# Optimization experiments

Measured on AMD Instinct MI355X. Metric: run time of the kernel, lower is better.

## Reference

```python
import jax, jax.numpy as jnp
import numpy as np

D, NH, DH, DHR, DC = 2048, 16, 128, 64, 1024
B, L = 2, 2048
EPS = 1e-6


def _rms(x, w):
    return x * jax.lax.rsqrt(jnp.mean(x * x, axis=-1, keepdims=True) + EPS) * w


def _rope_tables(seq_len, dim, dtype):
    inv_freq = 1.0 / (10000.0 ** (jnp.arange(0, dim, 2, dtype=jnp.float32) / dim))
    freqs = jnp.arange(seq_len, dtype=jnp.float32)[:, None] * inv_freq[None, :]  # [L, dim/2]
    emb = jnp.concatenate([freqs, freqs], axis=-1)                               # [L, dim]
    return jnp.cos(emb).astype(dtype), jnp.sin(emb).astype(dtype)


def _apply_rope(x, cos, sin):
    # x: [B, H, L, dhr]
    half = x.shape[-1] // 2
    x1, x2 = x[..., :half], x[..., half:]
    rot = jnp.concatenate([-x2, x1], axis=-1)
    return x * cos[None, None] + rot * sin[None, None]


def setup_inputs() -> dict:
    key = jax.random.key(0)
    ks = jax.random.split(key, 14)
    s = 0.02
    inp = {
        "x": jax.random.normal(ks[0], (B, L, D), dtype=jnp.float32),
        "W_DKV": jax.random.normal(ks[1], (D, DC), dtype=jnp.float32) * s,
        "kv_norm_w": 1.0 + 0.01 * jax.random.normal(ks[2], (DC,), dtype=jnp.float32),
        "W_UK": jax.random.normal(ks[3], (DC, NH * DH), dtype=jnp.float32) * s,
        "W_UV": jax.random.normal(ks[4], (DC, NH * DH), dtype=jnp.float32) * s,
        "W_DQ": jax.random.normal(ks[5], (D, DC), dtype=jnp.float32) * s,
        "q_norm_w": 1.0 + 0.01 * jax.random.normal(ks[6], (DC,), dtype=jnp.float32),
        "W_UQ": jax.random.normal(ks[7], (DC, 2 * NH * DH), dtype=jnp.float32) * s,
        "W_QR": jax.random.normal(ks[8], (DC, 2 * NH * DHR), dtype=jnp.float32) * s,
        "W_KR": jax.random.normal(ks[9], (D, DHR), dtype=jnp.float32) * s,
        "W_lambda_w": jax.random.normal(ks[10], (D, NH), dtype=jnp.float32) * s,
        "W_lambda_b": jax.random.normal(ks[11], (NH,), dtype=jnp.float32) * s,
        "W_out": jax.random.normal(ks[12], (D, D), dtype=jnp.float32) * s,
    }
    return inp


def reference(x, W_DKV, kv_norm_w, W_UK, W_UV, W_DQ, q_norm_w, W_UQ, W_QR,
              W_KR, W_lambda_w, W_lambda_b, W_out):
    Bx, Lx, Dx = x.shape
    nh, dh, dhr = NH, DH, DHR
    dq = dh + dhr  # per-head query/key dim after decoupled-RoPE concat (192)
    scale = 1.0 / jnp.sqrt(jnp.asarray(dq, dtype=x.dtype))

    # MLA KV path
    c_kv = _rms(x @ W_DKV, kv_norm_w)                                   # [B,L,dc]
    k_c = (c_kv @ W_UK).reshape(Bx, Lx, nh, dh).transpose(0, 2, 1, 3)    # [B,nh,L,dh]
    v = (c_kv @ W_UV).reshape(Bx, Lx, nh, dh).transpose(0, 2, 1, 3)      # [B,nh,L,dh]

    # MLA Q path (doubled heads for Diff V2)
    c_q = _rms(x @ W_DQ, q_norm_w)                                       # [B,L,dcq]
    q_c = (c_q @ W_UQ).reshape(Bx, Lx, 2 * nh, dh).transpose(0, 2, 1, 3)  # [B,2nh,L,dh]

    # Decoupled RoPE
    cos, sin = _rope_tables(Lx, dhr, x.dtype)
    q_r = _apply_rope((c_q @ W_QR).reshape(Bx, Lx, 2 * nh, dhr).transpose(0, 2, 1, 3), cos, sin)
    k_r = _apply_rope((x @ W_KR).reshape(Bx, Lx, 1, dhr).transpose(0, 2, 1, 3), cos, sin)  # [B,1,L,dhr]

    q = jnp.concatenate([q_c, q_r], axis=-1)                             # [B,2nh,L,dq]
    k = jnp.concatenate([k_c, jnp.broadcast_to(k_r, (Bx, nh, Lx, dhr))], axis=-1)  # [B,nh,L,dq]

    # repeat_interleave(2) on K/V == pairing two consecutive Q heads with one K/V head
    qp = q.reshape(Bx, nh, 2, Lx, dq)                                    # [B,nh,2,L,dq]
    scores = jnp.einsum('bnpld,bnmd->bnplm', qp, k) * scale              # [B,nh,2,L,L]
    causal = jnp.tril(jnp.ones((Lx, Lx), dtype=bool))
    scores = jnp.where(causal[None, None, None], scores, jnp.finfo(scores.dtype).min)
    p = jax.nn.softmax(scores, axis=-1)
    attn = jnp.einsum('bnplm,bnmd->bnpld', p, v)                         # [B,nh,2,L,dh]

    attn1, attn2 = attn[:, :, 0], attn[:, :, 1]                          # [B,nh,L,dh]
    lam = jax.nn.sigmoid(x @ W_lambda_w + W_lambda_b)                    # [B,L,nh]
    lam = lam.transpose(0, 2, 1)[..., None]                              # [B,nh,L,1]
    out = (attn1 - lam * attn2).transpose(0, 2, 1, 3).reshape(Bx, Lx, Dx)
    return out @ W_out
```

## Files before the change

### kernel.cpp

```cpp
#include <hip/hip_runtime.h>
#include <cstddef>
#include <cstdint>


namespace {

constexpr int kDC = 1024, kDim = 2048;
constexpr float kScale = 0.07216878364870323f;
constexpr int kTA = 2128;

typedef __bf16 bf16x8 __attribute__((ext_vector_type(8)));
typedef float f32x4 __attribute__((ext_vector_type(4)));

__device__ __forceinline__ unsigned short f2bf(float f) {
  __bf16 h = (__bf16)f;
  return __builtin_bit_cast(unsigned short, h);
}
__device__ __forceinline__ float bf2f(unsigned short h) {
  union { unsigned int u; float f; } v; v.u = ((unsigned int)h) << 16;
  return v.f;
}
__device__ __forceinline__ f32x4 mfma16(bf16x8 a, bf16x8 b, f32x4 c) {
  return __builtin_amdgcn_mfma_f32_16x16x32_bf16(a, b, c, 0, 0, 0);
}
__device__ __forceinline__ void gl_lds16(const void* g, void* l) {
  __builtin_amdgcn_global_load_lds(
      (const __attribute__((address_space(1))) unsigned int*)g,
      (__attribute__((address_space(3))) unsigned int*)l, 16, 0, 0);
}
__device__ __forceinline__ void wait_lgkm0() {
  asm volatile("s_waitcnt lgkmcnt(0)" ::: "memory");
}

__global__ __launch_bounds__(256) void conv_bf16_kernel(const float* __restrict__ in,
                                                        unsigned short* __restrict__ out, int n4) {
  int e = blockIdx.x * 256 + threadIdx.x;
  if (e >= n4) return;
  float4 v = reinterpret_cast<const float4*>(in)[e];
  uint2 pk;
  pk.x = (unsigned int)f2bf(v.x) | ((unsigned int)f2bf(v.y) << 16);
  pk.y = (unsigned int)f2bf(v.z) | ((unsigned int)f2bf(v.w) << 16);
  reinterpret_cast<uint2*>(out)[e] = pk;
}

__global__ __launch_bounds__(256) void zero_bf16_kernel(unsigned short* __restrict__ out, int n8) {
  int e = blockIdx.x * 256 + threadIdx.x;
  if (e >= n8) return;
  reinterpret_cast<uint4*>(out)[e] = uint4{0, 0, 0, 0};
}

__global__ __launch_bounds__(256) void transpose_conv_kernel(const float* __restrict__ in,
                                                             unsigned short* __restrict__ out,
                                                             int K, int N) {
  __shared__ float t[32][33];
  int n0 = blockIdx.x * 32, k0 = blockIdx.y * 32;
  int tx = threadIdx.x & 31, ty = threadIdx.x >> 5;
#pragma unroll
  for (int i = 0; i < 4; i++) t[ty + i * 8][tx] = in[(size_t)(k0 + ty + i * 8) * N + n0 + tx];
  __syncthreads();
#pragma unroll
  for (int i = 0; i < 4; i++)
    out[(size_t)(n0 + ty + i * 8) * K + k0 + tx] = f2bf(t[tx][ty + i * 8]);
}

__global__ __launch_bounds__(256) void lamw_transpose_kernel(const float* __restrict__ in,
                                                             unsigned short* __restrict__ out) {
  int e = blockIdx.x * 256 + threadIdx.x;
  if (e >= 16 * 2048) return;
  int k = e & 2047, n = e >> 11;
  out[(size_t)(2112 + n) * 2048 + k] = f2bf(in[(size_t)k * 16 + n]);
}

template <int MODE>
__device__ __forceinline__ void epi_store(void* dst, void* dst2, int gr, int gc, int N, float v) {
  if (MODE == 0) {
    reinterpret_cast<float*>(dst)[(size_t)gr * N + gc] = v;
  } else if (MODE == 4) {
    if (gc < kTA) reinterpret_cast<float*>(dst)[(size_t)gr * kTA + gc] = v;
  } else if (MODE == 5) {
    int bb = gr >> 11, l = gr & 2047;
    unsigned short hv = f2bf(v);
    if (gc < 2048) {
      int h = gc >> 7, d2 = gc & 127;
      int d2s = d2 ^ ((l & 7) << 3);
      reinterpret_cast<unsigned short*>(dst)[((size_t)((bb * 16 + h) * 2048 + l)) * 192 + d2s] = hv;
    } else {
      int g2 = gc - 2048, h = g2 >> 7, d2 = g2 & 127;
      int ls = l ^ (((d2 >> 1) & 3) << 3);
      reinterpret_cast<unsigned short*>(dst2)[((size_t)((bb * 16 + h) * 128 + d2)) * 2048 + ls] = hv;
    }
  } else if (MODE == 6) {
    int bb = gr >> 11, l = gr & 2047;
    if (gc < 4096) {
      int h2 = gc >> 7, d2 = gc & 127;
      reinterpret_cast<unsigned short*>(dst)[((size_t)((bb * 32 + h2) * 2048 + l)) * 192 + d2] =
          f2bf(v * kScale);
    } else {
      reinterpret_cast<unsigned short*>(dst2)[(size_t)gr * 2048 + (gc - 4096)] = f2bf(v);
    }
  }
}

template <int MODE>
__global__ __launch_bounds__(256) void gemm128_kernel(const unsigned short* __restrict__ A,
                                                      const unsigned short* __restrict__ Bt,
                                                      void* __restrict__ dst, void* __restrict__ dst2,
                                                      int M, int N, int K) {
  __shared__ unsigned short lds_a[128 * 32];
  __shared__ unsigned short lds_b[128 * 32];
  int tid = threadIdx.x, lane = tid & 63, w = tid >> 6;
  int quad = lane >> 4, l16 = lane & 15;
  int wr = w >> 1, wc = w & 1;
  int mbase = blockIdx.y * 128, nbase = blockIdx.x * 128;
  f32x4 acc[4][4] = {};
  int srow0 = tid >> 2, skoff = (tid & 3) * 8;
  const size_t a_base = (size_t)(mbase + srow0) * K + skoff;
  const size_t b_base = (size_t)(nbase + srow0) * K + skoff;
  unsigned short* lba0 = &lds_a[(size_t)(w * 64) * 8];
  unsigned short* lba1 = &lds_a[(size_t)(256 + w * 64) * 8];
  unsigned short* lbb0 = &lds_b[(size_t)(w * 64) * 8];
  unsigned short* lbb1 = &lds_b[(size_t)(256 + w * 64) * 8];
  for (int k0 = 0; k0 < K; k0 += 32) {
    __syncthreads();
    gl_lds16(&A[a_base + k0], lba0);
    gl_lds16(&A[a_base + (size_t)64 * K + k0], lba1);
    gl_lds16(&Bt[b_base + k0], lbb0);
    gl_lds16(&Bt[b_base + (size_t)64 * K + k0], lbb1);
    __syncthreads();
    bf16x8 af[4], bfr[4];
#pragma unroll
    for (int i = 0; i < 4; i++) {
      af[i] = *reinterpret_cast<const bf16x8*>(&lds_a[(wr * 64 + i * 16 + l16) * 32 + quad * 8]);
      bfr[i] = *reinterpret_cast<const bf16x8*>(&lds_b[(wc * 64 + i * 16 + l16) * 32 + quad * 8]);
    }
#pragma unroll
    for (int i = 0; i < 4; i++)
#pragma unroll
      for (int j = 0; j < 4; j++) acc[i][j] = mfma16(af[i], bfr[j], acc[i][j]);
  }
#pragma unroll
  for (int i = 0; i < 4; i++)
#pragma unroll
    for (int j = 0; j < 4; j++)
#pragma unroll
      for (int r = 0; r < 4; r++) {
        int gr = mbase + wr * 64 + i * 16 + quad * 4 + r;
        int gc = nbase + wc * 64 + j * 16 + l16;
        epi_store<MODE>(dst, dst2, gr, gc, N, acc[i][j][r]);
      }
}

__global__ __launch_bounds__(256) void rms_kernel(const float* __restrict__ in,
                                                  const float* __restrict__ w,
                                                  unsigned short* __restrict__ out, int colOff) {
  int row = blockIdx.x, tid = threadIdx.x;
  float4 v = reinterpret_cast<const float4*>(in + (size_t)row * kTA + colOff)[tid];
  float ss = v.x * v.x + v.y * v.y + v.z * v.z + v.w * v.w;
  ss += __shfl_xor(ss, 1); ss += __shfl_xor(ss, 2); ss += __shfl_xor(ss, 4);
  ss += __shfl_xor(ss, 8); ss += __shfl_xor(ss, 16); ss += __shfl_xor(ss, 32);
  __shared__ float red[4];
  if ((tid & 63) == 0) red[tid >> 6] = ss;
  __syncthreads();
  float tot = red[0] + red[1] + red[2] + red[3];
  float rs = rsqrtf(tot * (1.0f / kDC) + 1e-6f);
  float4 wv = reinterpret_cast<const float4*>(w)[tid];
  uint2 pk;
  pk.x = (unsigned int)f2bf(v.x * rs * wv.x) | ((unsigned int)f2bf(v.y * rs * wv.y) << 16);
  pk.y = (unsigned int)f2bf(v.z * rs * wv.z) | ((unsigned int)f2bf(v.w * rs * wv.w) << 16);
  reinterpret_cast<uint2*>(out)[(size_t)row * 256 + tid] = pk;
}

__device__ __forceinline__ float rope_val(float x1, float x2, int j, int l) {
  int i = j & 31;
  float inv_freq = powf(10000.0f, -(float)i * (1.0f / 32.0f));
  float ang = (float)l * inv_freq;
  float cv = cosf(ang), sv = sinf(ang);
  float rot = (j < 32) ? -x2 : x2;
  return x1 * cv + rot * sv;
}

__global__ __launch_bounds__(256) void rope_q_kernel(const unsigned short* __restrict__ qr_raw,
                                                     unsigned short* __restrict__ q_all) {
  size_t e = (size_t)blockIdx.x * 256 + threadIdx.x;
  int j = (int)(e & 63);
  int h2 = (int)((e >> 6) & 31);
  int bl = (int)(e >> 11);
  int l = bl & 2047, b = bl >> 11;
  float x1 = bf2f(qr_raw[(size_t)bl * 2048 + h2 * 64 + j]);
  float x2 = bf2f(qr_raw[(size_t)bl * 2048 + h2 * 64 + (j ^ 32)]);
  float val = rope_val(x1, x2, j, l) * kScale;
  q_all[((size_t)((b * 32 + h2) * 2048 + l)) * 192 + 128 + j] = f2bf(val);
}

__global__ __launch_bounds__(256) void rope_k_kernel(const float* __restrict__ tmpAll,
                                                     unsigned short* __restrict__ k_all) {
  size_t e = (size_t)blockIdx.x * 256 + threadIdx.x;
  int j = (int)(e & 63);
  int bl = (int)(e >> 6);
  int l = bl & 2047, b = bl >> 11;
  float x1 = tmpAll[(size_t)bl * kTA + 2048 + j];
  float x2 = tmpAll[(size_t)bl * kTA + 2048 + (j ^ 32)];
  unsigned short hv = f2bf(rope_val(x1, x2, j, l));
  int js = j ^ ((l & 7) << 3);
#pragma unroll
  for (int h = 0; h < 16; h++)
    k_all[((size_t)((b * 16 + h) * 2048 + l)) * 192 + 128 + js] = hv;
}

__global__ __launch_bounds__(256) void lam_fin_kernel(const float* __restrict__ tmpAll,
                                                      const float* __restrict__ bl_,
                                                      float* __restrict__ lam) {
  int e = blockIdx.x * 256 + threadIdx.x;
  if (e >= 4096 * 16) return;
  int n = e & 15, row = e >> 4;
  float z = tmpAll[(size_t)row * kTA + 2112 + n] + bl_[n];
  lam[e] = 1.f / (1.f + __expf(-z));
}

__global__ __launch_bounds__(256, 3) void attn3_kernel(const unsigned short* __restrict__ q_all,
                                                       const unsigned short* __restrict__ k_all,
                                                       const unsigned short* __restrict__ v_allT,
                                                       unsigned short* __restrict__ attn_o) {
  __shared__ unsigned short lds_k[2][32 * 192];
  __shared__ unsigned short lds_v[2][128 * 32];
  __shared__ unsigned short lds_p[8 * 640];
  __shared__ unsigned short lds_ones[16 * 32];
  int n = blockIdx.x, qp = blockIdx.y, b = blockIdx.z;
  int tid = threadIdx.x, lane = tid & 63, w = tid >> 6, quad = lane >> 4, l16 = lane & 15;
  const unsigned short* k_head = k_all + ((size_t)(b * 16 + n) * 2048) * 192;
  const unsigned short* v_head = v_allT + ((size_t)(b * 16 + n) * 128) * 2048;

  for (int idx = tid; idx < 512; idx += 256)
    lds_ones[idx] = (idx < 32) ? (unsigned short)0x3F80 : (unsigned short)0;

  unsigned short* pw0 = &lds_p[(w * 2 + 0) * 640];
  unsigned short* pw1 = &lds_p[(w * 2 + 1) * 640];

  auto stage = [&](int pos0, int buf) {
    const unsigned short* kg = k_head + (size_t)pos0 * 192 + w * 1536 + lane * 8;
    unsigned short* kl = &lds_k[buf][w * 1536];
    gl_lds16(kg, kl);
    gl_lds16(kg + 512, kl + 512);
    gl_lds16(kg + 1024, kl + 1024);
    const unsigned short* vg =
        v_head + (size_t)(w * 32 + (lane >> 2)) * 2048 + pos0 + (lane & 3) * 8;
    unsigned short* vl = &lds_v[buf][w * 1024];
    gl_lds16(vg, vl);
    gl_lds16(vg + (size_t)16 * 2048, vl + 512);
  };

#pragma unroll 1
  for (int phase = 0; phase < 2; ++phase) {
    int qt = phase ? qp : (31 - qp);
    const unsigned short* q0_row =
        q_all + ((size_t)(b * 32 + 2 * n) * 2048 + qt * 64 + w * 16 + l16) * 192;
    const unsigned short* q1_row = q0_row + (size_t)2048 * 192;

    bf16x8 qf0[6], qf1[6];
#pragma unroll
    for (int ks = 0; ks < 6; ks++) {
      qf0[ks] = *reinterpret_cast<const bf16x8*>(&q0_row[ks * 32 + quad * 8]);
      qf1[ks] = *reinterpret_cast<const bf16x8*>(&q1_row[ks * 32 + quad * 8]);
    }

    f32x4 acc0[9] = {}, acc1[9] = {};
    int qlo = qt * 64 + w * 16;
    int nt = 2 * qt + 2;

    stage(0, 0);
    for (int kt = 0; kt < nt; kt++) {
      int cur = kt & 1;
      int pos0 = kt * 32;
      __syncthreads();
      if (kt + 1 < nt) stage((kt + 1) * 32, cur ^ 1);
      if (pos0 <= qlo + 15) {
        const unsigned short* kb = &lds_k[cur][0];
        const unsigned short* vb = &lds_v[cur][0];
        bool needmask = (pos0 + 31 > qlo);
        int ksw = (l16 & 7) << 3;
        int vsw = (l16 >> 1) & 3;
#pragma unroll
        for (int j = 0; j < 2; j++) {
          f32x4 s0 = {}, s1 = {};
#pragma unroll
          for (int ks = 0; ks < 6; ks++) {
            bf16x8 bK = *reinterpret_cast<const bf16x8*>(
                &kb[(j * 16 + l16) * 192 + ((ks * 32 + quad * 8) ^ ksw)]);
            s0 = mfma16(qf0[ks], bK, s0);
            s1 = mfma16(qf1[ks], bK, s1);
          }
#pragma unroll
          for (int r = 0; r < 4; r++) {
            bool msk = needmask && (pos0 + j * 16 + l16 > qlo + quad * 4 + r);
            float p0 = msk ? 0.f : __expf(s0[r]);
            float p1 = msk ? 0.f : __expf(s1[r]);
            pw0[(quad * 4 + r) * 40 + j * 16 + l16] = f2bf(p0);
            pw1[(quad * 4 + r) * 40 + j * 16 + l16] = f2bf(p1);
          }
        }
        wait_lgkm0();
        bf16x8 pf0 = *reinterpret_cast<const bf16x8*>(&pw0[l16 * 40 + quad * 8]);
        bf16x8 pf1 = *reinterpret_cast<const bf16x8*>(&pw1[l16 * 40 + quad * 8]);
#pragma unroll
        for (int dt = 0; dt < 8; dt++) {
          bf16x8 vf = *reinterpret_cast<const bf16x8*>(
              &vb[(dt * 16 + l16) * 32 + ((quad ^ vsw) * 8)]);
          acc0[dt] = mfma16(pf0, vf, acc0[dt]);
          acc1[dt] = mfma16(pf1, vf, acc1[dt]);
        }
        bf16x8 vone = *reinterpret_cast<const bf16x8*>(&lds_ones[l16 * 32 + quad * 8]);
        acc0[8] = mfma16(pf0, vone, acc0[8]);
        acc1[8] = mfma16(pf1, vone, acc1[8]);
      }
    }

    unsigned short* o0 = attn_o + ((size_t)(b * 32 + 2 * n) * 2048 + qt * 64 + w * 16) * 128;
    unsigned short* o1 = o0 + (size_t)2048 * 128;
#pragma unroll
    for (int r = 0; r < 4; r++) {
      float li0 = __shfl(acc0[8][r], lane & 48);
      float li1 = __shfl(acc1[8][r], lane & 48);
      float inv0 = 1.f / li0, inv1 = 1.f / li1;
      int row = quad * 4 + r;
#pragma unroll
      for (int dt = 0; dt < 8; dt++) {
        o0[(size_t)row * 128 + dt * 16 + l16] = f2bf(acc0[dt][r] * inv0);
        o1[(size_t)row * 128 + dt * 16 + l16] = f2bf(acc1[dt][r] * inv1);
      }
    }
  }
}

__global__ __launch_bounds__(256) void combine_kernel(const unsigned short* __restrict__ attn_o,
                                                      const float* __restrict__ lam,
                                                      unsigned short* __restrict__ out) {
  size_t e = (size_t)blockIdx.x * 256 + threadIdx.x;
  int c8 = (int)(e & 255);
  int bl = (int)(e >> 8);
  int n = c8 >> 4, dd = (c8 & 15) * 8;
  int b = bl >> 11, l = bl & 2047;
  size_t base = ((size_t)((b * 32 + n * 2) * 2048 + l)) * 128 + dd;
  uint4 a1 = *reinterpret_cast<const uint4*>(attn_o + base);
  uint4 a2 = *reinterpret_cast<const uint4*>(attn_o + base + (size_t)2048 * 128);
  float lm = lam[(size_t)bl * 16 + n];
  unsigned int r[4];
  const unsigned int* p1 = &a1.x;
  const unsigned int* p2 = &a2.x;
#pragma unroll
  for (int i = 0; i < 4; i++) {
    float lo = bf2f((unsigned short)(p1[i] & 0xFFFF)) - lm * bf2f((unsigned short)(p2[i] & 0xFFFF));
    float hi = bf2f((unsigned short)(p1[i] >> 16)) - lm * bf2f((unsigned short)(p2[i] >> 16));
    r[i] = (unsigned int)f2bf(lo) | ((unsigned int)f2bf(hi) << 16);
  }
  *reinterpret_cast<uint4*>(out + e * 8) = uint4{r[0], r[1], r[2], r[3]};
}

}

extern "C" void kernel_launch(void* const* d_in, const int* in_sizes, int n_in,
                              void* d_out, int out_size, void* d_ws, size_t ws_size,
                              hipStream_t stream) {
  const float* x      = (const float*)d_in[0];
  const float* W_DKV  = (const float*)d_in[1];
  const float* kvnw   = (const float*)d_in[2];
  const float* W_UK   = (const float*)d_in[3];
  const float* W_UV   = (const float*)d_in[4];
  const float* W_DQ   = (const float*)d_in[5];
  const float* qnw    = (const float*)d_in[6];
  const float* W_UQ   = (const float*)d_in[7];
  const float* W_QR   = (const float*)d_in[8];
  const float* W_KR   = (const float*)d_in[9];
  const float* W_lw   = (const float*)d_in[10];
  const float* W_lb   = (const float*)d_in[11];
  const float* W_out  = (const float*)d_in[12];
  float* out = (float*)d_out;

  char* ws = (char*)d_ws;
  size_t off = 0;
  auto alloc = [&](size_t bytes) { char* p = ws + off; off += (bytes + 255) & ~(size_t)255; return p; };
  unsigned short* xb     = (unsigned short*)alloc((size_t)4096 * 2048 * 2);
  unsigned short* wd_cat = (unsigned short*)alloc((size_t)2176 * 2048 * 2);
  unsigned short* wu_cat = (unsigned short*)alloc((size_t)4096 * 1024 * 2);
  unsigned short* wuqr   = (unsigned short*)alloc((size_t)6144 * 1024 * 2);
  unsigned short* wout   = (unsigned short*)alloc((size_t)2048 * 2048 * 2);
  unsigned short* ckv    = (unsigned short*)alloc((size_t)4096 * 1024 * 2);
  unsigned short* cq     = (unsigned short*)alloc((size_t)4096 * 1024 * 2);
  unsigned short* k_all  = (unsigned short*)alloc((size_t)2 * 16 * 2048 * 192 * 2);
  unsigned short* v_allT = (unsigned short*)alloc((size_t)2 * 16 * 128 * 2048 * 2);
  unsigned short* q_all  = (unsigned short*)alloc((size_t)2 * 32 * 2048 * 192 * 2);
  unsigned short* attn_o = (unsigned short*)alloc((size_t)2 * 32 * 2048 * 128 * 2);
  unsigned short* attn_b = (unsigned short*)alloc((size_t)4096 * 2048 * 2);
  float* lam             = (float*)alloc((size_t)4096 * 16 * 4);
  float* tmpAll          = (float*)alloc((size_t)4096 * kTA * 4);
  unsigned short* tmpB   = (unsigned short*)tmpAll;
  (void)ws_size; (void)in_sizes; (void)n_in; (void)out_size;

  hipLaunchKernelGGL(conv_bf16_kernel, dim3(8192), dim3(256), 0, stream, x, xb, 2097152);
  hipLaunchKernelGGL(transpose_conv_kernel, dim3(32, 64), dim3(256), 0, stream, W_DKV, wd_cat, 2048, 1024);
  hipLaunchKernelGGL(transpose_conv_kernel, dim3(32, 64), dim3(256), 0, stream, W_DQ,
                     wd_cat + (size_t)1024 * 2048, 2048, 1024);
  hipLaunchKernelGGL(transpose_conv_kernel, dim3(2, 64), dim3(256), 0, stream, W_KR,
                     wd_cat + (size_t)2048 * 2048, 2048, 64);
  hipLaunchKernelGGL(lamw_transpose_kernel, dim3(128), dim3(256), 0, stream, W_lw, wd_cat);
  hipLaunchKernelGGL(zero_bf16_kernel, dim3(48), dim3(256), 0, stream,
                     wd_cat + (size_t)2128 * 2048, 12288);
  hipLaunchKernelGGL(transpose_conv_kernel, dim3(64, 32), dim3(256), 0, stream, W_UK, wu_cat, 1024, 2048);
  hipLaunchKernelGGL(transpose_conv_kernel, dim3(64, 32), dim3(256), 0, stream, W_UV,
                     wu_cat + (size_t)2048 * 1024, 1024, 2048);
  hipLaunchKernelGGL(transpose_conv_kernel, dim3(128, 32), dim3(256), 0, stream, W_UQ, wuqr, 1024, 4096);
  hipLaunchKernelGGL(transpose_conv_kernel, dim3(64, 32), dim3(256), 0, stream, W_QR,
                     wuqr + (size_t)4096 * 1024, 1024, 2048);
  hipLaunchKernelGGL(transpose_conv_kernel, dim3(64, 64), dim3(256), 0, stream, W_out, wout, 2048, 2048);

  hipLaunchKernelGGL(gemm128_kernel<4>, dim3(17, 32), dim3(256), 0, stream,
                     xb, wd_cat, tmpAll, (void*)nullptr, 4096, 2176, 2048);
  hipLaunchKernelGGL(rms_kernel, dim3(4096), dim3(256), 0, stream, tmpAll, kvnw, ckv, 0);
  hipLaunchKernelGGL(rms_kernel, dim3(4096), dim3(256), 0, stream, tmpAll, qnw, cq, 1024);
  hipLaunchKernelGGL(rope_k_kernel, dim3(1024), dim3(256), 0, stream, tmpAll, k_all);
  hipLaunchKernelGGL(lam_fin_kernel, dim3(256), dim3(256), 0, stream, tmpAll, W_lb, lam);

  hipLaunchKernelGGL(gemm128_kernel<5>, dim3(32, 32), dim3(256), 0, stream,
                     ckv, wu_cat, k_all, v_allT, 4096, 4096, 1024);
  hipLaunchKernelGGL(gemm128_kernel<6>, dim3(48, 32), dim3(256), 0, stream,
                     cq, wuqr, q_all, tmpB, 4096, 6144, 1024);
  hipLaunchKernelGGL(rope_q_kernel, dim3(32768), dim3(256), 0, stream, tmpB, q_all);

  hipLaunchKernelGGL(attn3_kernel, dim3(16, 16, 2), dim3(256), 0, stream,
                     q_all, k_all, v_allT, attn_o);

  hipLaunchKernelGGL(combine_kernel, dim3(4096), dim3(256), 0, stream, attn_o, lam, attn_b);
  hipLaunchKernelGGL(gemm128_kernel<0>, dim3(16, 32), dim3(256), 0, stream,
                     attn_b, wout, out, (void*)nullptr, 4096, 2048, 2048);
}
```

Before: 677.9 us.

## Split paired query heads across blocks and read V directly from global

The attention kernel now gives each block a single query head instead of both heads of a K/V pair, which doubles the grid and halves the per-block accumulator registers. Occupancy is raised to 4 blocks per SIMD. V fragments are loaded straight from global memory into registers rather than staged through LDS, so the V layout swizzle in the GEMM epilogue is removed. The trade-off is that K/V traffic doubles, because each K/V head is now read by two blocks, and the V loads are no longer asynchronous LDS copies overlapped with compute.

```diff
diff --git a/kernel.cpp b/kernel.cpp
--- a/kernel.cpp
+++ b/kernel.cpp
@@ -86,8 +86,7 @@
       reinterpret_cast<unsigned short*>(dst)[((size_t)((bb * 16 + h) * 2048 + l)) * 192 + d2s] = hv;
     } else {
       int g2 = gc - 2048, h = g2 >> 7, d2 = g2 & 127;
-      int ls = l ^ (((d2 >> 1) & 3) << 3);
-      reinterpret_cast<unsigned short*>(dst2)[((size_t)((bb * 16 + h) * 128 + d2)) * 2048 + ls] = hv;
+      reinterpret_cast<unsigned short*>(dst2)[((size_t)((bb * 16 + h) * 128 + d2)) * 2048 + l] = hv;
     }
   } else if (MODE == 6) {
     int bb = gr >> 11, l = gr & 2047;
@@ -217,116 +216,99 @@
   lam[e] = 1.f / (1.f + __expf(-z));
 }
 
-__global__ __launch_bounds__(256, 3) void attn3_kernel(const unsigned short* __restrict__ q_all,
+__global__ __launch_bounds__(256, 4) void attn4_kernel(const unsigned short* __restrict__ q_all,
                                                        const unsigned short* __restrict__ k_all,
                                                        const unsigned short* __restrict__ v_allT,
                                                        unsigned short* __restrict__ attn_o) {
   __shared__ unsigned short lds_k[2][32 * 192];
-  __shared__ unsigned short lds_v[2][128 * 32];
-  __shared__ unsigned short lds_p[8 * 640];
+  __shared__ unsigned short lds_p[4 * 640];
   __shared__ unsigned short lds_ones[16 * 32];
-  int n = blockIdx.x, qp = blockIdx.y, b = blockIdx.z;
+  int n = blockIdx.x, qp = blockIdx.y, zz = blockIdx.z;
+  int b = zz >> 1, var = zz & 1;
   int tid = threadIdx.x, lane = tid & 63, w = tid >> 6, quad = lane >> 4, l16 = lane & 15;
   const unsigned short* k_head = k_all + ((size_t)(b * 16 + n) * 2048) * 192;
   const unsigned short* v_head = v_allT + ((size_t)(b * 16 + n) * 128) * 2048;
+  int hq = b * 32 + 2 * n + var;
 
   for (int idx = tid; idx < 512; idx += 256)
     lds_ones[idx] = (idx < 32) ? (unsigned short)0x3F80 : (unsigned short)0;
-
-  unsigned short* pw0 = &lds_p[(w * 2 + 0) * 640];
-  unsigned short* pw1 = &lds_p[(w * 2 + 1) * 640];
-
-  auto stage = [&](int pos0, int buf) {
+  __syncthreads();
+
+  unsigned short* pw = &lds_p[w * 640];
+  const unsigned short* v_lane = v_head + (size_t)l16 * 2048 + quad * 8;
+
+  auto stageK = [&](int pos0, int buf) {
     const unsigned short* kg = k_head + (size_t)pos0 * 192 + w * 1536 + lane * 8;
     unsigned short* kl = &lds_k[buf][w * 1536];
     gl_lds16(kg, kl);
     gl_lds16(kg + 512, kl + 512);
     gl_lds16(kg + 1024, kl + 1024);
-    const unsigned short* vg =
-        v_head + (size_t)(w * 32 + (lane >> 2)) * 2048 + pos0 + (lane & 3) * 8;
-    unsigned short* vl = &lds_v[buf][w * 1024];
-    gl_lds16(vg, vl);
-    gl_lds16(vg + (size_t)16 * 2048, vl + 512);
   };
 
 #pragma unroll 1
   for (int phase = 0; phase < 2; ++phase) {
     int qt = phase ? qp : (31 - qp);
-    const unsigned short* q0_row =
-        q_all + ((size_t)(b * 32 + 2 * n) * 2048 + qt * 64 + w * 16 + l16) * 192;
-    const unsigned short* q1_row = q0_row + (size_t)2048 * 192;
-
-    bf16x8 qf0[6], qf1[6];
-#pragma unroll
-    for (int ks = 0; ks < 6; ks++) {
-      qf0[ks] = *reinterpret_cast<const bf16x8*>(&q0_row[ks * 32 + quad * 8]);
-      qf1[ks] = *reinterpret_cast<const bf16x8*>(&q1_row[ks * 32 + quad * 8]);
-    }
-
-    f32x4 acc0[9] = {}, acc1[9] = {};
+    const unsigned short* q_row =
+        q_all + ((size_t)hq * 2048 + qt * 64 + w * 16 + l16) * 192;
+
+    bf16x8 qf[6];
+#pragma unroll
+    for (int ks = 0; ks < 6; ks++)
+      qf[ks] = *reinterpret_cast<const bf16x8*>(&q_row[ks * 32 + quad * 8]);
+
+    f32x4 acc[9] = {};
     int qlo = qt * 64 + w * 16;
     int nt = 2 * qt + 2;
 
-    stage(0, 0);
+    stageK(0, 0);
     for (int kt = 0; kt < nt; kt++) {
       int cur = kt & 1;
       int pos0 = kt * 32;
       __syncthreads();
-      if (kt + 1 < nt) stage((kt + 1) * 32, cur ^ 1);
+      if (kt + 1 < nt) stageK((kt + 1) * 32, cur ^ 1);
       if (pos0 <= qlo + 15) {
         const unsigned short* kb = &lds_k[cur][0];
-        const unsigned short* vb = &lds_v[cur][0];
+        bf16x8 vf[8];
+        const unsigned short* vg = v_lane + pos0;
+#pragma unroll
+        for (int dt = 0; dt < 8; dt++)
+          vf[dt] = *reinterpret_cast<const bf16x8*>(&vg[(size_t)dt * 16 * 2048]);
         bool needmask = (pos0 + 31 > qlo);
         int ksw = (l16 & 7) << 3;
-        int vsw = (l16 >> 1) & 3;
 #pragma unroll
         for (int j = 0; j < 2; j++) {
-          f32x4 s0 = {}, s1 = {};
+          f32x4 s = {};
 #pragma unroll
           for (int ks = 0; ks < 6; ks++) {
             bf16x8 bK = *reinterpret_cast<const bf16x8*>(
                 &kb[(j * 16 + l16) * 192 + ((ks * 32 + quad * 8) ^ ksw)]);
-            s0 = mfma16(qf0[ks], bK, s0);
-            s1 = mfma16(qf1[ks], bK, s1);
+            s = mfma16(qf[ks], bK, s);
           }
 #pragma unroll
           for (int r = 0; r < 4; r++) {
             bool msk = needmask && (pos0 + j * 16 + l16 > qlo + quad * 4 + r);
-            float p0 = msk ? 0.f : __expf(s0[r]);
-            float p1 = msk ? 0.f : __expf(s1[r]);
-            pw0[(quad * 4 + r) * 40 + j * 16 + l16] = f2bf(p0);
-            pw1[(quad * 4 + r) * 40 + j * 16 + l16] = f2bf(p1);
+            float p = msk ? 0.f : __expf(s[r]);
+            pw[(quad * 4 + r) * 40 + j * 16 + l16] = f2bf(p);
           }
         }
         wait_lgkm0();
-        bf16x8 pf0 = *reinterpret_cast<const bf16x8*>(&pw0[l16 * 40 + quad * 8]);
-        bf16x8 pf1 = *reinterpret_cast<const bf16x8*>(&pw1[l16 * 40 + quad * 8]);
-#pragma unroll
-        for (int dt = 0; dt < 8; dt++) {
-          bf16x8 vf = *reinterpret_cast<const bf16x8*>(
-              &vb[(dt * 16 + l16) * 32 + ((quad ^ vsw) * 8)]);
-          acc0[dt] = mfma16(pf0, vf, acc0[dt]);
-          acc1[dt] = mfma16(pf1, vf, acc1[dt]);
-        }
+        bf16x8 pf = *reinterpret_cast<const bf16x8*>(&pw[l16 * 40 + quad * 8]);
+#pragma unroll
+        for (int dt = 0; dt < 8; dt++) acc[dt] = mfma16(pf, vf[dt], acc[dt]);
         bf16x8 vone = *reinterpret_cast<const bf16x8*>(&lds_ones[l16 * 32 + quad * 8]);
-        acc0[8] = mfma16(pf0, vone, acc0[8]);
-        acc1[8] = mfma16(pf1, vone, acc1[8]);
+        acc[8] = mfma16(pf, vone, acc[8]);
       }
     }
 
-    unsigned short* o0 = attn_o + ((size_t)(b * 32 + 2 * n) * 2048 + qt * 64 + w * 16) * 128;
-    unsigned short* o1 = o0 + (size_t)2048 * 128;
+    unsigned short* o = attn_o + ((size_t)hq * 2048 + qt * 64 + w * 16) * 128;
 #pragma unroll
     for (int r = 0; r < 4; r++) {
-      float li0 = __shfl(acc0[8][r], lane & 48);
-      float li1 = __shfl(acc1[8][r], lane & 48);
-      float inv0 = 1.f / li0, inv1 = 1.f / li1;
+      float li = __shfl(acc[8][r], lane & 48);
+      float inv = 1.f / li;
       int row = quad * 4 + r;
 #pragma unroll
-      for (int dt = 0; dt < 8; dt++) {
-        o0[(size_t)row * 128 + dt * 16 + l16] = f2bf(acc0[dt][r] * inv0);
-        o1[(size_t)row * 128 + dt * 16 + l16] = f2bf(acc1[dt][r] * inv1);
-      }
+      for (int dt = 0; dt < 8; dt++)
+        o[(size_t)row * 128 + dt * 16 + l16] = f2bf(acc[dt][r] * inv);
     }
   }
 }
@@ -425,7 +407,7 @@
                      cq, wuqr, q_all, tmpB, 4096, 6144, 1024);
   hipLaunchKernelGGL(rope_q_kernel, dim3(32768), dim3(256), 0, stream, tmpB, q_all);
 
-  hipLaunchKernelGGL(attn3_kernel, dim3(16, 16, 2), dim3(256), 0, stream,
+  hipLaunchKernelGGL(attn4_kernel, dim3(16, 16, 4), dim3(256), 0, stream,
                      q_all, k_all, v_allT, attn_o);
 
   hipLaunchKernelGGL(combine_kernel, dim3(4096), dim3(256), 0, stream, attn_o, lam, attn_b);
```

Result: slower. 797.3 us (+17.6%).
